# Optimization experiments

Hardware: AMD Instinct MI355X
Metric: run time of the kernel (lower is better)

## Reference

```python
import jax, jax.numpy as jnp
import numpy as np

N = 30000          # num nodes
E = 480000         # num edges (avg degree 16)
K = 3              # Chebyshev filter order
IN = 128           # input feature dim
LAMBDA_MAX = 2.0   # PyG default spectral bound
DIMS = [IN, 16, 32, 64, 128, 256, 512]


def setup_inputs() -> dict:
    key = jax.random.key(0)
    ks = jax.random.split(key, 20)
    inp = {
        "x": jax.random.normal(ks[0], (N, IN), dtype=jnp.float32),
        "edge_index": jax.random.randint(ks[1], (2, E), 0, N, dtype=jnp.int32),
        "edge_weight": jax.random.uniform(ks[2], (E,), dtype=jnp.float32),
        "batch": jnp.arange(N, dtype=jnp.int32),  # each node its own graph -> pooling is identity
    }
    for i in range(6):
        fi, fo = DIMS[i], DIMS[i + 1]
        scale = 1.0 / np.sqrt(fi * K)
        inp[f"W{i+1}"] = jax.random.normal(ks[3 + 2 * i], (K, fi, fo), dtype=jnp.float32) * scale
        inp[f"b{i+1}"] = jnp.zeros((fo,), dtype=jnp.float32)
    inp["fc_w"] = jax.random.normal(ks[16], (512, 3), dtype=jnp.float32) * 0.05
    inp["fc_b"] = jnp.zeros((3,), dtype=jnp.float32)
    return inp


def _cheb_conv(x, row, col, w_off, diag, W, b):
    """ChebConv with rw-normalized, rescaled Laplacian Lhat = 2L/lmax - I.
    Lhat @ v = scatter(w_off * v[row] -> col) + diag * v."""
    def lmv(v):
        return jax.ops.segment_sum(w_off[:, None] * v[row], col, num_segments=N) + diag * v
    Tx0 = x
    out = Tx0 @ W[0]
    Tx1 = lmv(x)
    out = out + Tx1 @ W[1]
    for k in range(2, W.shape[0]):
        Tx2 = 2.0 * lmv(Tx1) - Tx0
        out = out + Tx2 @ W[k]
        Tx0, Tx1 = Tx1, Tx2
    return out + b


def _forward(x, edge_index, edge_weight, batch, Ws, bs, fc_w, fc_b):
    row, col = edge_index[0], edge_index[1]
    # random-walk Laplacian L = I - D^{-1} A, then Lhat = 2L/lmax - I
    deg = jax.ops.segment_sum(edge_weight, row, num_segments=N)
    deg_inv = jnp.where(deg > 0, 1.0 / deg, 0.0)
    w_off = -(2.0 / LAMBDA_MAX) * deg_inv[row] * edge_weight   # off-diagonal entries of Lhat
    diag = 2.0 / LAMBDA_MAX - 1.0                               # diagonal entry of Lhat (0 for lmax=2)
    h = x
    for W, b in zip(Ws, bs):
        h = _cheb_conv(h, row, col, w_off, diag, W, b)
        h = jax.ops.segment_max(h, batch, num_segments=N)  # global_max_pool; identity since batch=arange
        h = jax.nn.softplus(h)
    return h @ fc_w + fc_b


def reference(x, edge_index, edge_weight, batch, W1, b1, W2, b2, W3, b3, W4, b4, W5, b5, W6, b6, fc_w, fc_b):
    Ws = [W1, W2, W3, W4, W5, W6]
    bs = [b1, b2, b3, b4, b5, b6]
    return _forward(x, edge_index, edge_weight, batch, Ws, bs, fc_w, fc_b)
```

## Files before the change

### kernel.cpp

```cpp
#include <hip/hip_runtime.h>
#include <math.h>
#include <stdint.h>

#define NN 30000
#define EE 480000
#define MPAD 30080
#define NPAD 30720
#define NB_HIST 32
#define CHUNK 15000

typedef __attribute__((ext_vector_type(8))) short short8;
typedef __attribute__((ext_vector_type(4))) float floatx4;

__device__ __forceinline__ float b2f(ushort u) {
    union { uint u; float f; } c; c.u = ((uint)u) << 16; return c.f;
}
__device__ __forceinline__ ushort f2b(float f) {
    union { float f; uint u; } c; c.f = f;
    uint u = c.u;
    uint r = (u + 0x7FFFu + ((u >> 16) & 1u)) >> 16;
    return (ushort)r;
}
__device__ __forceinline__ float softplus_f(float x) {
    float a = fabsf(x) * 1.44269504f;
    float t = __builtin_amdgcn_exp2f(-a);
    float l = __builtin_amdgcn_logf(1.f + t);
    return fmaxf(x, 0.f) + 0.69314718f * l;
}

__device__ __forceinline__ void gld_lds16(const void* g, void* lds) {
    __builtin_amdgcn_global_load_lds(
        (__attribute__((address_space(1))) void*)(uintptr_t)(g),
        (__attribute__((address_space(3))) void*)(uint32_t)(uintptr_t)(lds),
        16, 0, 0);
}

__device__ __forceinline__ void barrier_raw() {
    __asm__ volatile("s_barrier" ::: "memory");
}
template <int N>
__device__ __forceinline__ void waitcnt_vm() {
    if constexpr (N == 0) __asm__ volatile("s_waitcnt vmcnt(0)" ::: "memory");
    else if constexpr (N == 2) __asm__ volatile("s_waitcnt vmcnt(2)" ::: "memory");
    else if constexpr (N == 3) __asm__ volatile("s_waitcnt vmcnt(3)" ::: "memory");
    else if constexpr (N == 4) __asm__ volatile("s_waitcnt vmcnt(4)" ::: "memory");
    else if constexpr (N == 8) __asm__ volatile("s_waitcnt vmcnt(8)" ::: "memory");
}


__global__ __launch_bounds__(256) void pre1_fused(
        const int* __restrict__ row, const int* __restrict__ col,
        const float* __restrict__ ew,
        int* __restrict__ Hpart, float* __restrict__ Dpart,
        const float* __restrict__ x, ushort* __restrict__ xb,
        const float* __restrict__ W1, const float* __restrict__ W2,
        const float* __restrict__ W3, const float* __restrict__ W4,
        const float* __restrict__ W5, const float* __restrict__ W6,
        ushort* __restrict__ B1, ushort* __restrict__ B2,
        ushort* __restrict__ B3, ushort* __restrict__ B4,
        ushort* __restrict__ B5, ushort* __restrict__ B6) {
    __shared__ int hist[NPAD];
    int b = blockIdx.x;
    int t = threadIdx.x;
    if (b < NB_HIST) {
        int e0 = b * CHUNK, e1 = e0 + CHUNK;
        #pragma unroll
        for (int i = 0; i < NPAD / 1024; ++i)
            *(int4*)(&hist[(i * 256 + t) * 4]) = make_int4(0, 0, 0, 0);
        __syncthreads();
        int e = e0 + t;
        for (; e + 2048 <= e1; e += 2048) {
            int c0 = col[e],        c1 = col[e + 256];
            int c2 = col[e + 512],  c3 = col[e + 768];
            int c4 = col[e + 1024], c5 = col[e + 1280];
            int c6 = col[e + 1536], c7 = col[e + 1792];
            atomicAdd(&hist[c0], 1); atomicAdd(&hist[c1], 1);
            atomicAdd(&hist[c2], 1); atomicAdd(&hist[c3], 1);
            atomicAdd(&hist[c4], 1); atomicAdd(&hist[c5], 1);
            atomicAdd(&hist[c6], 1); atomicAdd(&hist[c7], 1);
        }
        for (; e < e1; e += 256) atomicAdd(&hist[col[e]], 1);
        __syncthreads();
        #pragma unroll
        for (int i = 0; i < NPAD / 1024; ++i)
            *(int4*)(&Hpart[(size_t)b * NPAD + (i * 256 + t) * 4]) =
                *(const int4*)(&hist[(i * 256 + t) * 4]);
        __syncthreads();
        float* histf = (float*)hist;
        #pragma unroll
        for (int i = 0; i < NPAD / 1024; ++i)
            *(float4*)(&histf[(i * 256 + t) * 4]) = make_float4(0.f, 0.f, 0.f, 0.f);
        __syncthreads();
        e = e0 + t;
        for (; e + 1024 <= e1; e += 1024) {
            int r0 = row[e],       r1 = row[e + 256];
            int r2 = row[e + 512], r3 = row[e + 768];
            float w0 = ew[e],       w1 = ew[e + 256];
            float w2 = ew[e + 512], w3 = ew[e + 768];
            atomicAdd(&histf[r0], w0); atomicAdd(&histf[r1], w1);
            atomicAdd(&histf[r2], w2); atomicAdd(&histf[r3], w3);
        }
        for (; e < e1; e += 256) atomicAdd(&histf[row[e]], ew[e]);
        __syncthreads();
        #pragma unroll
        for (int i = 0; i < NPAD / 1024; ++i)
            *(float4*)(&Dpart[(size_t)b * NPAD + (i * 256 + t) * 4]) =
                *(const float4*)(&histf[(i * 256 + t) * 4]);
    } else if (b < NB_HIST + 480) {
        int id = b - NB_HIST;
        #pragma unroll
        for (int i = 0; i < 8; ++i) {
            int idx = id * 2048 + i * 256 + t;
            if (idx < NN * 128 / 4) {
                float4 v = *(const float4*)(x + (size_t)idx * 4);
                ushort4 o;
                o.x = f2b(v.x); o.y = f2b(v.y); o.z = f2b(v.z); o.w = f2b(v.w);
                *(ushort4*)(xb + (size_t)idx * 4) = o;
            }
        }
    } else {
        int id = b - NB_HIST - 480;
        #pragma unroll
        for (int i = 0; i < 8; ++i) {
            int idx = id * 2048 + i * 256 + t;
            if (idx < 6144) {
                int r = idx >> 7, k = idx & 127;
                int j = r >> 4, n = r & 15;
                B1[idx] = f2b(W1[(j * 128 + k) * 16 + n]);
            } else if (idx < 8192) {
                int tt = idx - 6144; int n = tt >> 6, k = tt & 63;
                B2[tt] = f2b(k < 48 ? W2[k * 32 + n] : 0.f);
            } else if (idx < 14336) {
                int tt = idx - 8192; int n = tt / 96, k = tt - n * 96;
                B3[tt] = f2b(W3[k * 64 + n]);
            } else if (idx < 38912) {
                int tt = idx - 14336; int n = tt / 192, k = tt - n * 192;
                B4[tt] = f2b(W4[k * 128 + n]);
            } else if (idx < 137216) {
                int tt = idx - 38912; int n = tt / 384, k = tt - n * 384;
                B5[tt] = f2b(W5[k * 256 + n]);
            } else if (idx < 530432) {
                int tt = idx - 137216; int n = tt / 768, k = tt - n * 768;
                B6[tt] = f2b(W6[k * 512 + n]);
            }
        }
    }
}

__global__ __launch_bounds__(256) void col_reduce(
        int* __restrict__ Hpart, const float* __restrict__ Dpart,
        int* __restrict__ counts, float* __restrict__ deg) {
    int c = blockIdx.x * 256 + threadIdx.x;
    int run = 0;
    #pragma unroll
    for (int b = 0; b < NB_HIST; ++b) {
        int v = Hpart[(size_t)b * NPAD + c];
        Hpart[(size_t)b * NPAD + c] = run;
        run += v;
    }
    counts[c] = run;
    float s = 0.f;
    #pragma unroll
    for (int b = 0; b < NB_HIST; ++b) s += Dpart[(size_t)b * NPAD + c];
    deg[c] = s;
}

__global__ __launch_bounds__(1024) void scan_one(
        const int* __restrict__ counts, int* __restrict__ offs) {
    __shared__ int ws[16];
    int t = threadIdx.x;
    int wave = t >> 6, lane = t & 63;
    int base = t * 32;
    int c[32];
    int s = 0;
    if (base < NN) {
        #pragma unroll
        for (int g = 0; g < 8; ++g) {
            int4 v = *(const int4*)(counts + base + g * 4);
            c[g * 4 + 0] = v.x; c[g * 4 + 1] = v.y;
            c[g * 4 + 2] = v.z; c[g * 4 + 3] = v.w;
        }
        #pragma unroll
        for (int i = 0; i < 32; ++i) s += c[i];
    } else {
        #pragma unroll
        for (int i = 0; i < 32; ++i) c[i] = 0;
    }
    int incl = s;
    #pragma unroll
    for (int off = 1; off < 64; off <<= 1) {
        int xv = __shfl_up(incl, off);
        if (lane >= off) incl += xv;
    }
    if (lane == 63) ws[wave] = incl;
    __syncthreads();
    if (wave == 0) {
        int v = (lane < 16) ? ws[lane] : 0;
        #pragma unroll
        for (int off = 1; off < 16; off <<= 1) {
            int xv = __shfl_up(v, off);
            if (lane >= off) v += xv;
        }
        if (lane < 16) ws[lane] = v;
    }
    __syncthreads();
    int wbase = (wave == 0) ? 0 : ws[wave - 1];
    int run = wbase + incl - s;
    if (base < NN) {
        int o[32];
        #pragma unroll
        for (int i = 0; i < 32; ++i) { o[i] = run; run += c[i]; }
        #pragma unroll
        for (int g = 0; g < 8; ++g) {
            int4 v = make_int4(o[g * 4], o[g * 4 + 1], o[g * 4 + 2], o[g * 4 + 3]);
            *(int4*)(offs + base + g * 4) = v;
        }
    }
    if (t == 0) offs[NN] = EE;
}

template <int BN, bool ACT>
__device__ __forceinline__ void gemm_mfma_body(
        int bid, const ushort* __restrict__ A, int lda, int K,
        const ushort* __restrict__ Bt, const float* __restrict__ bias,
        ushort* __restrict__ Out, int ldo) {
    constexpr int BM = 128, BK = 32;
    constexpr int SM = 32;
    constexpr int FM = 2;
    constexpr int FN = BN / 16;
    constexpr int CB = BN / 16;
    constexpr int WAITN = (BN == 64) ? 3 : 2;
    __shared__ __align__(16) ushort As[2][BM][BK];
    __shared__ __align__(16) ushort Bs[2][BN][BK];
    int tid = threadIdx.x;
    int wv = tid >> 6, ln = tid & 63;
    int q = ln >> 4, r16 = ln & 15;
    int m0 = bid * BM;

    int lrow = ln >> 2;
    int gseg = (ln & 3) ^ ((ln >> 3) & 3);
    const ushort* Abase = A + (size_t)(m0 + lrow) * lda + gseg * 8;
    const ushort* Bbase = Bt + (size_t)lrow * K + gseg * 8;

    floatx4 acc[FM][FN];
    #pragma unroll
    for (int i = 0; i < FM; ++i)
        #pragma unroll
        for (int j = 0; j < FN; ++j) acc[i][j] = (floatx4){0.f, 0.f, 0.f, 0.f};

    int sw = (q ^ ((r16 >> 1) & 3)) * 8;
    int aoff[FM], boff[FN];
    #pragma unroll
    for (int i = 0; i < FM; ++i) aoff[i] = (wv * SM + i * 16 + r16) * BK + sw;
    #pragma unroll
    for (int j = 0; j < FN; ++j) boff[j] = (j * 16 + r16) * BK + sw;

    auto stage = [&](int b, int k0) {
        gld_lds16(Abase + (size_t)(wv * 16) * lda + k0, &As[b][wv * 16][0]);
        gld_lds16(Abase + (size_t)(64 + wv * 16) * lda + k0, &As[b][64 + wv * 16][0]);
        if constexpr (CB == 4) {
            gld_lds16(Bbase + (size_t)(wv * 16) * K + k0, &Bs[b][wv * 16][0]);
        } else {
            if (wv < CB) gld_lds16(Bbase + (size_t)(wv * 16) * K + k0, &Bs[b][wv * 16][0]);
        }
    };
    auto compute = [&](int b) {
        const ushort* ldsA = &As[b][0][0];
        const ushort* ldsB = &Bs[b][0][0];
        short8 af[FM], bf[FN];
        #pragma unroll
        for (int i = 0; i < FM; ++i) af[i] = *(const short8*)(ldsA + aoff[i]);
        #pragma unroll
        for (int j = 0; j < FN; ++j) bf[j] = *(const short8*)(ldsB + boff[j]);
        #pragma unroll
        for (int i = 0; i < FM; ++i)
            #pragma unroll
            for (int j = 0; j < FN; ++j)
                acc[i][j] = __builtin_amdgcn_mfma_f32_16x16x32_bf16(
                    af[i], bf[j], acc[i][j], 0, 0, 0);
    };

    int nIter = K / BK;
    stage(0, 0);
    for (int i = 0; i < nIter; ++i) {
        int cur = i & 1;
        barrier_raw();
        if (i + 1 < nIter) {
            stage(cur ^ 1, (i + 1) * BK);
            waitcnt_vm<WAITN>();
        } else {
            waitcnt_vm<0>();
        }
        barrier_raw();
        compute(cur);
    }
    #pragma unroll
    for (int i = 0; i < FM; ++i) {
        #pragma unroll
        for (int j = 0; j < FN; ++j) {
            int n = j * 16 + r16;
            float bv = ACT ? bias[n] : 0.f;
            #pragma unroll
            for (int r = 0; r < 4; ++r) {
                int m = m0 + wv * SM + i * 16 + q * 4 + r;
                float v = acc[i][j][r] + bv;
                Out[(size_t)m * ldo + n] = f2b(ACT ? softplus_f(v) : v);
            }
        }
    }
}

template <int BN, bool ACT = true>
__global__ __launch_bounds__(256) void gemm_mfma(
        const ushort* __restrict__ A, int lda, int K,
        const ushort* __restrict__ Bt,
        const float* __restrict__ bias,
        ushort* __restrict__ Out, int ldo) {
    gemm_mfma_body<BN, ACT>(blockIdx.x, A, lda, K, Bt, bias, Out, ldo);
}

__global__ __launch_bounds__(256) void pre2_fused(
        const int* __restrict__ row, const int* __restrict__ col,
        const float* __restrict__ ew, const float* __restrict__ deg,
        const int* __restrict__ offs, const int* __restrict__ Hpart,
        int2* __restrict__ csr_rw,
        const ushort* __restrict__ xb, const ushort* __restrict__ Bt1,
        ushort* __restrict__ Ybuf) {
    int b = blockIdx.x;
    if (b < NB_HIST) {
        __shared__ int cur[NPAD];
        int t = threadIdx.x;
        #pragma unroll
        for (int i = 0; i < NPAD / 1024; ++i) {
            int idx = (i * 256 + t) * 4;
            int4 o = *(const int4*)(offs + idx);
            int4 pfx = *(const int4*)(Hpart + (size_t)b * NPAD + idx);
            cur[idx + 0] = o.x + pfx.x;
            cur[idx + 1] = o.y + pfx.y;
            cur[idx + 2] = o.z + pfx.z;
            cur[idx + 3] = o.w + pfx.w;
        }
        __syncthreads();
        int e0 = b * CHUNK, e1 = e0 + CHUNK;
        int e = e0 + t;
        for (; e + 1024 <= e1; e += 1024) {
            int r0 = row[e],       r1 = row[e + 256];
            int r2 = row[e + 512], r3 = row[e + 768];
            int c0 = col[e],       c1 = col[e + 256];
            int c2 = col[e + 512], c3 = col[e + 768];
            float w0 = ew[e],       w1 = ew[e + 256];
            float w2 = ew[e + 512], w3 = ew[e + 768];
            float d0 = deg[r0], d1 = deg[r1], d2 = deg[r2], d3 = deg[r3];
            float v0 = (d0 > 0.f) ? (-w0 / d0) : 0.f;
            float v1 = (d1 > 0.f) ? (-w1 / d1) : 0.f;
            float v2 = (d2 > 0.f) ? (-w2 / d2) : 0.f;
            float v3 = (d3 > 0.f) ? (-w3 / d3) : 0.f;
            int p0 = atomicAdd(&cur[c0], 1);
            int p1 = atomicAdd(&cur[c1], 1);
            int p2 = atomicAdd(&cur[c2], 1);
            int p3 = atomicAdd(&cur[c3], 1);
            csr_rw[p0] = make_int2(r0, __float_as_int(v0));
            csr_rw[p1] = make_int2(r1, __float_as_int(v1));
            csr_rw[p2] = make_int2(r2, __float_as_int(v2));
            csr_rw[p3] = make_int2(r3, __float_as_int(v3));
        }
        for (; e < e1; e += 256) {
            int r = row[e];
            float d = deg[r];
            float wv = (d > 0.f) ? (-ew[e] / d) : 0.f;
            int pos = atomicAdd(&cur[col[e]], 1);
            csr_rw[pos] = make_int2(r, __float_as_int(wv));
        }
    } else {
        gemm_mfma_body<48, false>(b - NB_HIST, xb, 128, 128, Bt1, nullptr,
                                  Ybuf, 48);
    }
}

template <int FI>
__global__ __launch_bounds__(256) void lmv_bf16(
        const ushort* __restrict__ A, ushort* __restrict__ Out,
        const ushort* __restrict__ Sub, int ldi, int ldo,
        const int* __restrict__ offs, const int2* __restrict__ rw,
        float scale, int N) {
    constexpr int NPW = 64 / FI;
    int wave = threadIdx.x >> 6;
    int lane = threadIdx.x & 63;
    int sub = lane / FI;
    int fbase = lane & (FI - 1);
    int node = blockIdx.x * (4 * NPW) + wave * NPW + sub;
    if (node >= N) return;
    int e0 = offs[node], e1 = offs[node + 1];
    float acc[4];
    #pragma unroll
    for (int c = 0; c < 4; ++c) acc[c] = 0.f;
    int e = e0;
    for (; e + 4 <= e1; e += 4) {
        int2 u0 = rw[e], u1 = rw[e + 1], u2 = rw[e + 2], u3 = rw[e + 3];
        acc[0] += __int_as_float(u0.y) * b2f(A[(size_t)u0.x * ldi + fbase]);
        acc[1] += __int_as_float(u1.y) * b2f(A[(size_t)u1.x * ldi + fbase]);
        acc[2] += __int_as_float(u2.y) * b2f(A[(size_t)u2.x * ldi + fbase]);
        acc[3] += __int_as_float(u3.y) * b2f(A[(size_t)u3.x * ldi + fbase]);
    }
    for (; e < e1; ++e) {
        int2 u = rw[e];
        acc[0] += __int_as_float(u.y) * b2f(A[(size_t)u.x * ldi + fbase]);
    }
    float a = (acc[0] + acc[1]) + (acc[2] + acc[3]);
    ushort* o = Out + (size_t)node * ldo + fbase;
    if (Sub) {
        const ushort* s = Sub + (size_t)node * ldo + fbase;
        *o = f2b(scale * a - b2f(*s));
    } else {
        *o = f2b(scale * a);
    }
}

__global__ __launch_bounds__(256) void lmv_l1_final(
        const ushort* __restrict__ Z,
        const ushort* __restrict__ Y,
        const float* __restrict__ b,
        ushort* __restrict__ Out,
        const int* __restrict__ offs, const int2* __restrict__ rw, int N) {
    int wave = threadIdx.x >> 6;
    int lane = threadIdx.x & 63;
    int sub = lane >> 4, f = lane & 15;
    int node = blockIdx.x * 16 + wave * 4 + sub;
    if (node >= N) return;
    int e0 = offs[node], e1 = offs[node + 1];
    const ushort* Z2 = Z + 16;
    float acc[4];
    #pragma unroll
    for (int c = 0; c < 4; ++c) acc[c] = 0.f;
    int e = e0;
    for (; e + 4 <= e1; e += 4) {
        int2 u0 = rw[e], u1 = rw[e + 1], u2 = rw[e + 2], u3 = rw[e + 3];
        acc[0] += __int_as_float(u0.y) * b2f(Z2[(size_t)u0.x * 32 + f]);
        acc[1] += __int_as_float(u1.y) * b2f(Z2[(size_t)u1.x * 32 + f]);
        acc[2] += __int_as_float(u2.y) * b2f(Z2[(size_t)u2.x * 32 + f]);
        acc[3] += __int_as_float(u3.y) * b2f(Z2[(size_t)u3.x * 32 + f]);
    }
    for (; e < e1; ++e) {
        int2 u = rw[e];
        acc[0] += __int_as_float(u.y) * b2f(Z2[(size_t)u.x * 32 + f]);
    }
    float z3 = (acc[0] + acc[1]) + (acc[2] + acc[3]);
    float y0 = b2f(Y[(size_t)node * 48 + f]);
    float y2 = b2f(Y[(size_t)node * 48 + 32 + f]);
    float z1 = b2f(Z[(size_t)node * 32 + f]);
    float v = y0 + z1 + 2.f * z3 - y2 + b[f];
    Out[(size_t)node * 64 + f] = f2b(softplus_f(v));
}

template <int LPG>
__global__ __launch_bounds__(256) void lmv_grp(
        const ushort* __restrict__ A, ushort* __restrict__ Out,
        const ushort* __restrict__ Sub, int ld,
        const int* __restrict__ offs, const int2* __restrict__ rw,
        float scale) {
    constexpr int EG = 64 / LPG;
    int node = blockIdx.x * 4 + (threadIdx.x >> 6);
    int lane = threadIdx.x & 63;
    int g = lane / LPG;
    int li = lane % LPG;
    int fbase = li * 4;
    int e0 = __builtin_amdgcn_readfirstlane(offs[node]);
    int e1 = __builtin_amdgcn_readfirstlane(offs[node + 1]);
    float a0[4], a1[4];
    #pragma unroll
    for (int j = 0; j < 4; ++j) { a0[j] = 0.f; a1[j] = 0.f; }
    int e = e0 + g;
    for (; e + EG < e1; e += 2 * EG) {
        int2 u0 = rw[e];
        int2 u1 = rw[e + EG];
        float w0 = __int_as_float(u0.y), w1 = __int_as_float(u1.y);
        ushort4 v0 = *(const ushort4*)(A + (size_t)u0.x * ld + fbase);
        ushort4 v1 = *(const ushort4*)(A + (size_t)u1.x * ld + fbase);
        a0[0] += w0 * b2f(v0.x); a0[1] += w0 * b2f(v0.y);
        a0[2] += w0 * b2f(v0.z); a0[3] += w0 * b2f(v0.w);
        a1[0] += w1 * b2f(v1.x); a1[1] += w1 * b2f(v1.y);
        a1[2] += w1 * b2f(v1.z); a1[3] += w1 * b2f(v1.w);
    }
    if (e < e1) {
        int2 u = rw[e];
        float w = __int_as_float(u.y);
        ushort4 v = *(const ushort4*)(A + (size_t)u.x * ld + fbase);
        a0[0] += w * b2f(v.x); a0[1] += w * b2f(v.y);
        a0[2] += w * b2f(v.z); a0[3] += w * b2f(v.w);
    }
    #pragma unroll
    for (int j = 0; j < 4; ++j) {
        float a = a0[j] + a1[j];
        #pragma unroll
        for (int off = LPG; off < 64; off <<= 1)
            a += __shfl_xor(a, off);
        a0[j] = a;
    }
    if (g == 0) {
        ushort* o = Out + (size_t)node * ld + fbase;
        ushort4 w;
        if (Sub) {
            ushort4 s = *(const ushort4*)(Sub + (size_t)node * ld + fbase);
            w.x = f2b(scale * a0[0] - b2f(s.x));
            w.y = f2b(scale * a0[1] - b2f(s.y));
            w.z = f2b(scale * a0[2] - b2f(s.z));
            w.w = f2b(scale * a0[3] - b2f(s.w));
        } else {
            w.x = f2b(scale * a0[0]); w.y = f2b(scale * a0[1]);
            w.z = f2b(scale * a0[2]); w.w = f2b(scale * a0[3]);
        }
        *(ushort4*)o = w;
    }
}

template <int VEC>
__global__ __launch_bounds__(256) void lmv_vec(
        const ushort* __restrict__ A, ushort* __restrict__ Out,
        const ushort* __restrict__ Sub, int ld,
        const int* __restrict__ offs, const int2* __restrict__ rw,
        float scale) {
    constexpr int CH = 8;
    int node = blockIdx.x * 4 + (threadIdx.x >> 6);
    int lane = threadIdx.x & 63;
    int fbase = lane * VEC;
    int e0 = __builtin_amdgcn_readfirstlane(offs[node]);
    int e1 = __builtin_amdgcn_readfirstlane(offs[node + 1]);
    float acc[CH][VEC];
    #pragma unroll
    for (int c = 0; c < CH; ++c)
        #pragma unroll
        for (int v = 0; v < VEC; ++v) acc[c][v] = 0.f;
    int e = e0;
    for (; e + CH <= e1; e += CH) {
        #pragma unroll
        for (int c = 0; c < CH; ++c) {
            int2 u = rw[e + c];
            int r = u.x;
            float we = __int_as_float(u.y);
            const ushort* pr = A + (size_t)r * ld + fbase;
            if constexpr (VEC == 4) {
                ushort4 uu = *(const ushort4*)pr;
                acc[c][0] += we * b2f(uu.x); acc[c][1] += we * b2f(uu.y);
                acc[c][2] += we * b2f(uu.z); acc[c][3] += we * b2f(uu.w);
            } else if constexpr (VEC == 2) {
                ushort2 uu = *(const ushort2*)pr;
                acc[c][0] += we * b2f(uu.x); acc[c][1] += we * b2f(uu.y);
            } else {
                acc[c][0] += we * b2f(*pr);
            }
        }
    }
    for (; e < e1; ++e) {
        int c = e & (CH - 1);
        int2 u = rw[e];
        int r = u.x;
        float we = __int_as_float(u.y);
        const ushort* pr = A + (size_t)r * ld + fbase;
        if constexpr (VEC == 4) {
            ushort4 uu = *(const ushort4*)pr;
            acc[c][0] += we * b2f(uu.x); acc[c][1] += we * b2f(uu.y);
            acc[c][2] += we * b2f(uu.z); acc[c][3] += we * b2f(uu.w);
        } else if constexpr (VEC == 2) {
            ushort2 uu = *(const ushort2*)pr;
            acc[c][0] += we * b2f(uu.x); acc[c][1] += we * b2f(uu.y);
        } else {
            acc[c][0] += we * b2f(*pr);
        }
    }
    #pragma unroll
    for (int c = 1; c < CH; ++c)
        #pragma unroll
        for (int v = 0; v < VEC; ++v) acc[0][v] += acc[c][v];
    ushort* o = Out + (size_t)node * ld + fbase;
    if (Sub) {
        const ushort* s = Sub + (size_t)node * ld + fbase;
        ushort tmp[VEC];
        #pragma unroll
        for (int v = 0; v < VEC; ++v) tmp[v] = f2b(scale * acc[0][v] - b2f(s[v]));
        #pragma unroll
        for (int v = 0; v < VEC; ++v) o[v] = tmp[v];
    } else {
        #pragma unroll
        for (int v = 0; v < VEC; ++v) o[v] = f2b(scale * acc[0][v]);
    }
}

template <bool FC = false, int YB = 0>
__global__ __launch_bounds__(256) void gemm_bk64(
        const ushort* __restrict__ A, int lda, int K,
        const ushort* __restrict__ Bt,
        const float* __restrict__ bias,
        ushort* __restrict__ Out, int ldo,
        const float* __restrict__ fcw, float* __restrict__ fcout) {
    constexpr int BM = 128, BN = 128, BK = 64;
    __shared__ __align__(16) ushort As[2][BM][BK];
    __shared__ __align__(16) ushort Bs[2][BN][BK];
    int tid = threadIdx.x;
    int wv = tid >> 6, ln = tid & 63;
    int wm = wv & 1, wn = wv >> 1;
    int q = ln >> 4, r16 = ln & 15;
    int nwg = gridDim.x;
    int orig = blockIdx.x;
    int xcd = orig & 7;
    int qq = nwg >> 3, rr = nwg & 7;
    int wbase = (xcd < rr) ? xcd * (qq + 1) : rr * (qq + 1) + (xcd - rr) * qq;
    int wgid = wbase + (orig >> 3);
    int yb = wgid & ((1 << YB) - 1);
    int xb = wgid >> YB;
    int m0 = xb * BM;
    int n0 = yb * BN;

    int lrow8 = ln >> 3, slds = ln & 7;
    int gseg = slds ^ lrow8;
    const ushort* Abase = A + (size_t)(m0 + lrow8) * lda + gseg * 8;
    const ushort* Bbase = Bt + (size_t)(n0 + lrow8) * K + gseg * 8;

    floatx4 acc[4][4];
    #pragma unroll
    for (int i = 0; i < 4; ++i)
        #pragma unroll
        for (int j = 0; j < 4; ++j) acc[i][j] = (floatx4){0.f, 0.f, 0.f, 0.f};

    int r7 = r16 & 7;
    int aoff[2][4], boff[2][4];
    #pragma unroll
    for (int s = 0; s < 2; ++s) {
        int segp = ((s * 4 + q) ^ r7) * 8;
        #pragma unroll
        for (int i = 0; i < 4; ++i) {
            aoff[s][i] = (wm * 64 + i * 16 + r16) * BK + segp;
            boff[s][i] = (wn * 64 + i * 16 + r16) * BK + segp;
        }
    }

    auto stage = [&](int b, int k0) {
        #pragma unroll
        for (int g = 0; g < 4; ++g)
            gld_lds16(Abase + (size_t)(wv * 8 + g * 32) * lda + k0,
                      &As[b][wv * 8 + g * 32][0]);
        #pragma unroll
        for (int g = 0; g < 4; ++g)
            gld_lds16(Bbase + (size_t)(wv * 8 + g * 32) * K + k0,
                      &Bs[b][wv * 8 + g * 32][0]);
    };
    auto compute = [&](int b) {
        const ushort* ldsA = &As[b][0][0];
        const ushort* ldsB = &Bs[b][0][0];
        #pragma unroll
        for (int s = 0; s < 2; ++s) {
            short8 af[4], bf[4];
            #pragma unroll
            for (int i = 0; i < 4; ++i) af[i] = *(const short8*)(ldsA + aoff[s][i]);
            #pragma unroll
            for (int j = 0; j < 4; ++j) bf[j] = *(const short8*)(ldsB + boff[s][j]);
            #pragma unroll
            for (int i = 0; i < 4; ++i)
                #pragma unroll
                for (int j = 0; j < 4; ++j)
                    acc[i][j] = __builtin_amdgcn_mfma_f32_16x16x32_bf16(
                        af[i], bf[j], acc[i][j], 0, 0, 0);
        }
    };

    int nIter = K / BK;
    stage(0, 0);
    for (int i = 0; i < nIter; ++i) {
        int cur = i & 1;
        barrier_raw();
        if (i + 1 < nIter) {
            stage(cur ^ 1, (i + 1) * BK);
            waitcnt_vm<8>();
        } else {
            waitcnt_vm<0>();
        }
        barrier_raw();
        compute(cur);
    }

    if constexpr (FC) {
        int pb = yb * 2 + wn;
        #pragma unroll
        for (int i = 0; i < 4; ++i) {
            #pragma unroll
            for (int r = 0; r < 4; ++r) {
                float p0 = 0.f, p1 = 0.f, p2 = 0.f;
                #pragma unroll
                for (int j = 0; j < 4; ++j) {
                    int n = n0 + wn * 64 + j * 16 + r16;
                    float v = softplus_f(acc[i][j][r] + bias[n]);
                    p0 += v * fcw[n * 3 + 0];
                    p1 += v * fcw[n * 3 + 1];
                    p2 += v * fcw[n * 3 + 2];
                }
                #pragma unroll
                for (int off = 1; off < 16; off <<= 1) {
                    p0 += __shfl_xor(p0, off);
                    p1 += __shfl_xor(p1, off);
                    p2 += __shfl_xor(p2, off);
                }
                if (r16 == 0) {
                    int m = m0 + wm * 64 + i * 16 + q * 4 + r;
                    float* dst = fcout + ((size_t)pb * MPAD + m) * 3;
                    dst[0] = p0; dst[1] = p1; dst[2] = p2;
                }
            }
        }
    } else {
        #pragma unroll
        for (int i = 0; i < 4; ++i) {
            #pragma unroll
            for (int j = 0; j < 4; ++j) {
                int n = n0 + wn * 64 + j * 16 + r16;
                float bv = bias[n];
                #pragma unroll
                for (int r = 0; r < 4; ++r) {
                    int m = m0 + wm * 64 + i * 16 + q * 4 + r;
                    Out[(size_t)m * ldo + n] = f2b(softplus_f(acc[i][j][r] + bv));
                }
            }
        }
    }
}

__global__ __launch_bounds__(256) void fc_reduce(
        const float* __restrict__ part, const float* __restrict__ fcb,
        float* __restrict__ out) {
    int idx = blockIdx.x * blockDim.x + threadIdx.x;
    if (idx >= NN * 3) return;
    int c = idx - (idx / 3) * 3;
    float s = 0.f;
    #pragma unroll
    for (int pb = 0; pb < 8; ++pb)
        s += part[(size_t)pb * MPAD * 3 + idx];
    out[idx] = s + fcb[c];
}

static inline size_t align256(size_t x) { return (x + 255) & ~(size_t)255; }

extern "C" void kernel_launch(void* const* d_in, const int* in_sizes, int n_in,
                              void* d_out, int out_size, void* d_ws, size_t ws_size,
                              hipStream_t stream) {
    const float* x   = (const float*)d_in[0];
    const int*   ei  = (const int*)d_in[1];
    const float* ew  = (const float*)d_in[2];
    const float* W[6]  = { (const float*)d_in[4],  (const float*)d_in[6],
                           (const float*)d_in[8],  (const float*)d_in[10],
                           (const float*)d_in[12], (const float*)d_in[14] };
    const float* Bv[6] = { (const float*)d_in[5],  (const float*)d_in[7],
                           (const float*)d_in[9],  (const float*)d_in[11],
                           (const float*)d_in[13], (const float*)d_in[15] };
    const float* fc_w = (const float*)d_in[16];
    const float* fc_b = (const float*)d_in[17];
    float* out = (float*)d_out;

    const int* e_row = ei;
    const int* e_col = ei + EE;

    const int fi_arr[5]   = { 16, 32, 64, 128, 256 };
    const int fo_arr[5]   = { 32, 64, 128, 256, 512 };
    const int Kpad_arr[5] = { 64, 96, 192, 384, 768 };
    const int ldo_arr[5]  = { 96, 192, 384, 768, 512 };

    char* p = (char*)d_ws;
    float* deg    = (float*)p; p += align256((size_t)NPAD * 4);
    int*   counts = (int*)p;   p += align256((size_t)NPAD * 4);
    int*   offs   = (int*)p;   p += align256((size_t)(NPAD + 4) * 4);
    int*   Hpart  = (int*)p;   p += align256((size_t)NB_HIST * NPAD * 4);
    float* Dpart  = (float*)p; p += align256((size_t)NB_HIST * NPAD * 4);
    int2*  csr_rw = (int2*)p;  p += align256((size_t)EE * 8);
    ushort* Bt1   = (ushort*)p; p += align256((size_t)48 * 128 * 2);
    ushort* Bt[5];
    for (int L = 0; L < 5; ++L) {
        Bt[L] = (ushort*)p;
        p += align256((size_t)fo_arr[L] * Kpad_arr[L] * 2);
    }
    float* fcpart = (float*)p; p += align256((size_t)8 * MPAD * 3 * 4);
    ushort* xb   = (ushort*)p; p += align256((size_t)MPAD * 128 * 2);
    ushort* Ybuf = (ushort*)p; p += align256((size_t)MPAD * 48 * 2);
    ushort* Zbuf = (ushort*)p; p += align256((size_t)MPAD * 32 * 2);
    ushort* buf0 = (ushort*)p; p += align256((size_t)MPAD * 768 * 2);
    ushort* buf1 = (ushort*)p; p += align256((size_t)MPAD * 768 * 2);
    (void)ws_size; (void)n_in; (void)in_sizes; (void)out_size;


    pre1_fused<<<NB_HIST + 480 + 260, 256, 0, stream>>>(
        e_row, e_col, ew, Hpart, Dpart, x, xb,
        W[0], W[1], W[2], W[3], W[4], W[5],
        Bt1, Bt[0], Bt[1], Bt[2], Bt[3], Bt[4]);

    col_reduce<<<NPAD / 256, 256, 0, stream>>>(Hpart, Dpart, counts, deg);

    scan_one<<<1, 1024, 0, stream>>>(counts, offs);

    pre2_fused<<<NB_HIST + MPAD / 128, 256, 0, stream>>>(
        e_row, e_col, ew, deg, offs, Hpart, csr_rw, xb, Bt1, Ybuf);

    lmv_bf16<32><<<(NN + 7) / 8, 256, 0, stream>>>(
        Ybuf + 16, Zbuf, nullptr, 48, 32, offs, csr_rw, 1.0f, NN);
    lmv_l1_final<<<(NN + 15) / 16, 256, 0, stream>>>(
        Zbuf, Ybuf, Bv[0], buf1, offs, csr_rw, NN);

    ushort* Abuf[5] = { buf1, buf0, buf1, buf0, buf1 };
    ushort* Obuf[5] = { buf0, buf1, buf0, buf1, buf0 };

    for (int L = 0; L < 5; ++L) {
        int fi = fi_arr[L];
        int ldA = Kpad_arr[L];
        int ldO = ldo_arr[L];
        ushort* A = Abuf[L];
        ushort* O = Obuf[L];

        switch (fi) {
            case 16:
                lmv_bf16<16><<<(NN + 15) / 16, 256, 0, stream>>>(
                    A, A + fi, nullptr, ldA, ldA, offs, csr_rw, 1.0f, NN);
                lmv_bf16<16><<<(NN + 15) / 16, 256, 0, stream>>>(
                    A + fi, A + 2 * fi, A, ldA, ldA, offs, csr_rw, 2.0f, NN);
                break;
            case 32:
                lmv_bf16<32><<<(NN + 7) / 8, 256, 0, stream>>>(
                    A, A + fi, nullptr, ldA, ldA, offs, csr_rw, 1.0f, NN);
                lmv_bf16<32><<<(NN + 7) / 8, 256, 0, stream>>>(
                    A + fi, A + 2 * fi, A, ldA, ldA, offs, csr_rw, 2.0f, NN);
                break;
            case 64:
                lmv_grp<16><<<NN / 4, 256, 0, stream>>>(
                    A, A + fi, nullptr, ldA, offs, csr_rw, 1.0f);
                lmv_grp<16><<<NN / 4, 256, 0, stream>>>(
                    A + fi, A + 2 * fi, A, ldA, offs, csr_rw, 2.0f);
                break;
            case 128:
                lmv_grp<32><<<NN / 4, 256, 0, stream>>>(
                    A, A + fi, nullptr, ldA, offs, csr_rw, 1.0f);
                lmv_grp<32><<<NN / 4, 256, 0, stream>>>(
                    A + fi, A + 2 * fi, A, ldA, offs, csr_rw, 2.0f);
                break;
            default:
                lmv_vec<4><<<NN / 4, 256, 0, stream>>>(
                    A, A + fi, nullptr, ldA, offs, csr_rw, 1.0f);
                lmv_vec<4><<<NN / 4, 256, 0, stream>>>(
                    A + fi, A + 2 * fi, A, ldA, offs, csr_rw, 2.0f);
                break;
        }

        int K = Kpad_arr[L];
        switch (fo_arr[L]) {
            case 32:
                gemm_mfma<32><<<dim3(MPAD / 128), 256, 0, stream>>>(
                    A, ldA, K, Bt[L], Bv[L + 1], O, ldO);
                break;
            case 64:
                gemm_mfma<64><<<dim3(MPAD / 128), 256, 0, stream>>>(
                    A, ldA, K, Bt[L], Bv[L + 1], O, ldO);
                break;
            case 128:
                gemm_bk64<false, 0><<<dim3(MPAD / 128), 256, 0, stream>>>(
                    A, ldA, K, Bt[L], Bv[L + 1], O, ldO, nullptr, nullptr);
                break;
            case 256:
                gemm_bk64<false, 1><<<dim3(MPAD / 128 * 2), 256, 0, stream>>>(
                    A, ldA, K, Bt[L], Bv[L + 1], O, ldO, nullptr, nullptr);
                break;
            default:
                gemm_bk64<true, 2><<<dim3(MPAD / 128 * 4), 256, 0, stream>>>(
                    A, ldA, K, Bt[L], Bv[L + 1], nullptr, 0, fc_w, fcpart);
                break;
        }
    }

    fc_reduce<<<(NN * 3 + 255) / 256, 256, 0, stream>>>(fcpart, fc_b, out);
}
```

Measured before the change: 459.9 us.

## Split feature columns into 64-wide chunks pinned to XCDs for L2 locality

Replaces the vectorized per-node SpMM kernel for the 128- and 256-wide layers with a chunked kernel. Each 64-column slice of the feature matrix is assigned to a subset of XCDs via the block index modulo 8, so each XCD's L2 only caches a slice of the gathered rows. Edge list loads and output stores become nontemporal. This gives up vector loads (each lane now loads a single bf16) and per-node unrolling depth, and relies on the round-robin mapping of blocks to XCDs.

```diff
diff --git a/kernel.cpp b/kernel.cpp
--- a/kernel.cpp
+++ b/kernel.cpp
@@ -513,75 +513,56 @@
     }
 }
 
-template <int VEC>
-__global__ __launch_bounds__(256) void lmv_vec(
+template <int NCHUNK>
+__global__ __launch_bounds__(256) void lmv_chunk(
         const ushort* __restrict__ A, ushort* __restrict__ Out,
         const ushort* __restrict__ Sub, int ld,
         const int* __restrict__ offs, const int2* __restrict__ rw,
         float scale) {
-    constexpr int CH = 8;
-    int node = blockIdx.x * 4 + (threadIdx.x >> 6);
+    constexpr int XPC = 8 / NCHUNK;
+    int b = blockIdx.x;
+    int xcd = b & 7;
+    int chunk = xcd / XPC;
+    int rank = (b >> 3) * XPC + (xcd % XPC);
+    if (rank >= 1875) return;
+    int coff = chunk * 64;
+    int wave = threadIdx.x >> 6;
     int lane = threadIdx.x & 63;
-    int fbase = lane * VEC;
-    int e0 = __builtin_amdgcn_readfirstlane(offs[node]);
-    int e1 = __builtin_amdgcn_readfirstlane(offs[node + 1]);
-    float acc[CH][VEC];
-    #pragma unroll
-    for (int c = 0; c < CH; ++c)
-        #pragma unroll
-        for (int v = 0; v < VEC; ++v) acc[c][v] = 0.f;
-    int e = e0;
-    for (; e + CH <= e1; e += CH) {
-        #pragma unroll
-        for (int c = 0; c < CH; ++c) {
-            int2 u = rw[e + c];
-            int r = u.x;
-            float we = __int_as_float(u.y);
-            const ushort* pr = A + (size_t)r * ld + fbase;
-            if constexpr (VEC == 4) {
-                ushort4 uu = *(const ushort4*)pr;
-                acc[c][0] += we * b2f(uu.x); acc[c][1] += we * b2f(uu.y);
-                acc[c][2] += we * b2f(uu.z); acc[c][3] += we * b2f(uu.w);
-            } else if constexpr (VEC == 2) {
-                ushort2 uu = *(const ushort2*)pr;
-                acc[c][0] += we * b2f(uu.x); acc[c][1] += we * b2f(uu.y);
-            } else {
-                acc[c][0] += we * b2f(*pr);
-            }
-        }
-    }
-    for (; e < e1; ++e) {
-        int c = e & (CH - 1);
-        int2 u = rw[e];
-        int r = u.x;
-        float we = __int_as_float(u.y);
-        const ushort* pr = A + (size_t)r * ld + fbase;
-        if constexpr (VEC == 4) {
-            ushort4 uu = *(const ushort4*)pr;
-            acc[c][0] += we * b2f(uu.x); acc[c][1] += we * b2f(uu.y);
-            acc[c][2] += we * b2f(uu.z); acc[c][3] += we * b2f(uu.w);
-        } else if constexpr (VEC == 2) {
-            ushort2 uu = *(const ushort2*)pr;
-            acc[c][0] += we * b2f(uu.x); acc[c][1] += we * b2f(uu.y);
+    const ushort* Ac = A + coff + lane;
+    #pragma unroll
+    for (int nn = 0; nn < 4; ++nn) {
+        int node = rank * 16 + wave * 4 + nn;
+        int e0 = offs[node], e1 = offs[node + 1];
+        float ac0 = 0.f, ac1 = 0.f, ac2 = 0.f, ac3 = 0.f;
+        int e = e0;
+        for (; e + 4 <= e1; e += 4) {
+            long long q0 = __builtin_nontemporal_load((const long long*)(rw + e));
+            long long q1 = __builtin_nontemporal_load((const long long*)(rw + e + 1));
+            long long q2 = __builtin_nontemporal_load((const long long*)(rw + e + 2));
+            long long q3 = __builtin_nontemporal_load((const long long*)(rw + e + 3));
+            int r0 = (int)q0; float w0 = __int_as_float((int)(q0 >> 32));
+            int r1 = (int)q1; float w1 = __int_as_float((int)(q1 >> 32));
+            int r2 = (int)q2; float w2 = __int_as_float((int)(q2 >> 32));
+            int r3 = (int)q3; float w3 = __int_as_float((int)(q3 >> 32));
+            ac0 += w0 * b2f(Ac[(size_t)r0 * ld]);
+            ac1 += w1 * b2f(Ac[(size_t)r1 * ld]);
+            ac2 += w2 * b2f(Ac[(size_t)r2 * ld]);
+            ac3 += w3 * b2f(Ac[(size_t)r3 * ld]);
+        }
+        for (; e < e1; ++e) {
+            long long q = __builtin_nontemporal_load((const long long*)(rw + e));
+            int r = (int)q; float w = __int_as_float((int)(q >> 32));
+            ac0 += w * b2f(Ac[(size_t)r * ld]);
+        }
+        float a = (ac0 + ac1) + (ac2 + ac3);
+        ushort ov;
+        if (Sub) {
+            ushort sv = Sub[(size_t)node * ld + coff + lane];
+            ov = f2b(scale * a - b2f(sv));
         } else {
-            acc[c][0] += we * b2f(*pr);
-        }
-    }
-    #pragma unroll
-    for (int c = 1; c < CH; ++c)
-        #pragma unroll
-        for (int v = 0; v < VEC; ++v) acc[0][v] += acc[c][v];
-    ushort* o = Out + (size_t)node * ld + fbase;
-    if (Sub) {
-        const ushort* s = Sub + (size_t)node * ld + fbase;
-        ushort tmp[VEC];
-        #pragma unroll
-        for (int v = 0; v < VEC; ++v) tmp[v] = f2b(scale * acc[0][v] - b2f(s[v]));
-        #pragma unroll
-        for (int v = 0; v < VEC; ++v) o[v] = tmp[v];
-    } else {
-        #pragma unroll
-        for (int v = 0; v < VEC; ++v) o[v] = f2b(scale * acc[0][v]);
+            ov = f2b(scale * a);
+        }
+        __builtin_nontemporal_store(ov, Out + (size_t)node * ld + coff + lane);
     }
 }
 
@@ -830,15 +811,15 @@
                     A + fi, A + 2 * fi, A, ldA, offs, csr_rw, 2.0f);
                 break;
             case 128:
-                lmv_grp<32><<<NN / 4, 256, 0, stream>>>(
+                lmv_chunk<2><<<8 * 469, 256, 0, stream>>>(
                     A, A + fi, nullptr, ldA, offs, csr_rw, 1.0f);
-                lmv_grp<32><<<NN / 4, 256, 0, stream>>>(
+                lmv_chunk<2><<<8 * 469, 256, 0, stream>>>(
                     A + fi, A + 2 * fi, A, ldA, offs, csr_rw, 2.0f);
                 break;
             default:
-                lmv_vec<4><<<NN / 4, 256, 0, stream>>>(
+                lmv_chunk<4><<<8 * 938, 256, 0, stream>>>(
                     A, A + fi, nullptr, ldA, offs, csr_rw, 1.0f);
-                lmv_vec<4><<<NN / 4, 256, 0, stream>>>(
+                lmv_chunk<4><<<8 * 938, 256, 0, stream>>>(
                     A + fi, A + 2 * fi, A, ldA, offs, csr_rw, 2.0f);
                 break;
         }
```

After: 632.0 us. +37.4%, slower.

## Switch large GEMMs to 4-stage BK=32 pipelined LDS prefetch

Applied to the files above, without the earlier changes.

Replaces the double-buffered BK=64 GEMM with a four-buffer BK=32 pipeline that prefetches three k-steps ahead using direct global-to-LDS loads. The staging layout and XOR swizzle change to match the narrower 32-element rows. The aim is to hide global load latency with more loads in flight while keeping the same LDS footprint. The cost is twice as many barriers per unit of K and less MFMA work between syncs.

```diff
diff --git a/kernel.cpp b/kernel.cpp
--- a/kernel.cpp
+++ b/kernel.cpp
@@ -45,6 +45,7 @@
     else if constexpr (N == 3) __asm__ volatile("s_waitcnt vmcnt(3)" ::: "memory");
     else if constexpr (N == 4) __asm__ volatile("s_waitcnt vmcnt(4)" ::: "memory");
     else if constexpr (N == 8) __asm__ volatile("s_waitcnt vmcnt(8)" ::: "memory");
+    else if constexpr (N == 12) __asm__ volatile("s_waitcnt vmcnt(12)" ::: "memory");
 }
 
 
@@ -585,16 +586,16 @@
     }
 }
 
-template <bool FC = false, int YB = 0>
-__global__ __launch_bounds__(256) void gemm_bk64(
+template <bool FC, int YB>
+__global__ __launch_bounds__(256) void gemm_pipe(
         const ushort* __restrict__ A, int lda, int K,
         const ushort* __restrict__ Bt,
         const float* __restrict__ bias,
         ushort* __restrict__ Out, int ldo,
         const float* __restrict__ fcw, float* __restrict__ fcout) {
-    constexpr int BM = 128, BN = 128, BK = 64;
-    __shared__ __align__(16) ushort As[2][BM][BK];
-    __shared__ __align__(16) ushort Bs[2][BN][BK];
+    constexpr int BM = 128, BN = 128, BK = 32;
+    __shared__ __align__(16) ushort As[4][BM][BK];
+    __shared__ __align__(16) ushort Bs[4][BN][BK];
     int tid = threadIdx.x;
     int wv = tid >> 6, ln = tid & 63;
     int wm = wv & 1, wn = wv >> 1;
@@ -610,10 +611,10 @@
     int m0 = xb * BM;
     int n0 = yb * BN;
 
-    int lrow8 = ln >> 3, slds = ln & 7;
-    int gseg = slds ^ lrow8;
-    const ushort* Abase = A + (size_t)(m0 + lrow8) * lda + gseg * 8;
-    const ushort* Bbase = Bt + (size_t)(n0 + lrow8) * K + gseg * 8;
+    int lrow = ln >> 2;
+    int gseg = (ln & 3) ^ ((ln >> 3) & 3);
+    const ushort* Abase = A + (size_t)(m0 + lrow) * lda + gseg * 8;
+    const ushort* Bbase = Bt + (size_t)(n0 + lrow) * K + gseg * 8;
 
     floatx4 acc[4][4];
     #pragma unroll
@@ -621,55 +622,50 @@
         #pragma unroll
         for (int j = 0; j < 4; ++j) acc[i][j] = (floatx4){0.f, 0.f, 0.f, 0.f};
 
-    int r7 = r16 & 7;
-    int aoff[2][4], boff[2][4];
-    #pragma unroll
-    for (int s = 0; s < 2; ++s) {
-        int segp = ((s * 4 + q) ^ r7) * 8;
-        #pragma unroll
-        for (int i = 0; i < 4; ++i) {
-            aoff[s][i] = (wm * 64 + i * 16 + r16) * BK + segp;
-            boff[s][i] = (wn * 64 + i * 16 + r16) * BK + segp;
-        }
+    int sw = (q ^ ((r16 >> 1) & 3)) * 8;
+    int aoff[4], boff[4];
+    #pragma unroll
+    for (int i = 0; i < 4; ++i) {
+        aoff[i] = (wm * 64 + i * 16 + r16) * BK + sw;
+        boff[i] = (wn * 64 + i * 16 + r16) * BK + sw;
     }
 
     auto stage = [&](int b, int k0) {
-        #pragma unroll
-        for (int g = 0; g < 4; ++g)
-            gld_lds16(Abase + (size_t)(wv * 8 + g * 32) * lda + k0,
-                      &As[b][wv * 8 + g * 32][0]);
-        #pragma unroll
-        for (int g = 0; g < 4; ++g)
-            gld_lds16(Bbase + (size_t)(wv * 8 + g * 32) * K + k0,
-                      &Bs[b][wv * 8 + g * 32][0]);
+        gld_lds16(Abase + (size_t)(wv * 16) * lda + k0, &As[b][wv * 16][0]);
+        gld_lds16(Abase + (size_t)(64 + wv * 16) * lda + k0, &As[b][64 + wv * 16][0]);
+        gld_lds16(Bbase + (size_t)(wv * 16) * K + k0, &Bs[b][wv * 16][0]);
+        gld_lds16(Bbase + (size_t)(64 + wv * 16) * K + k0, &Bs[b][64 + wv * 16][0]);
     };
     auto compute = [&](int b) {
         const ushort* ldsA = &As[b][0][0];
         const ushort* ldsB = &Bs[b][0][0];
-        #pragma unroll
-        for (int s = 0; s < 2; ++s) {
-            short8 af[4], bf[4];
+        short8 af[4], bf[4];
+        #pragma unroll
+        for (int i = 0; i < 4; ++i) af[i] = *(const short8*)(ldsA + aoff[i]);
+        #pragma unroll
+        for (int j = 0; j < 4; ++j) bf[j] = *(const short8*)(ldsB + boff[j]);
+        #pragma unroll
+        for (int i = 0; i < 4; ++i)
             #pragma unroll
-            for (int i = 0; i < 4; ++i) af[i] = *(const short8*)(ldsA + aoff[s][i]);
-            #pragma unroll
-            for (int j = 0; j < 4; ++j) bf[j] = *(const short8*)(ldsB + boff[s][j]);
-            #pragma unroll
-            for (int i = 0; i < 4; ++i)
-                #pragma unroll
-                for (int j = 0; j < 4; ++j)
-                    acc[i][j] = __builtin_amdgcn_mfma_f32_16x16x32_bf16(
-                        af[i], bf[j], acc[i][j], 0, 0, 0);
-        }
+            for (int j = 0; j < 4; ++j)
+                acc[i][j] = __builtin_amdgcn_mfma_f32_16x16x32_bf16(
+                    af[i], bf[j], acc[i][j], 0, 0, 0);
     };
 
     int nIter = K / BK;
     stage(0, 0);
+    stage(1, BK);
+    stage(2, 2 * BK);
     for (int i = 0; i < nIter; ++i) {
-        int cur = i & 1;
+        int cur = i & 3;
         barrier_raw();
-        if (i + 1 < nIter) {
-            stage(cur ^ 1, (i + 1) * BK);
+        if (i + 3 < nIter) {
+            stage((i + 3) & 3, (i + 3) * BK);
+            waitcnt_vm<12>();
+        } else if (i + 2 < nIter) {
             waitcnt_vm<8>();
+        } else if (i + 1 < nIter) {
+            waitcnt_vm<4>();
         } else {
             waitcnt_vm<0>();
         }
@@ -854,15 +850,15 @@
                     A, ldA, K, Bt[L], Bv[L + 1], O, ldO);
                 break;
             case 128:
-                gemm_bk64<false, 0><<<dim3(MPAD / 128), 256, 0, stream>>>(
+                gemm_pipe<false, 0><<<dim3(MPAD / 128), 256, 0, stream>>>(
                     A, ldA, K, Bt[L], Bv[L + 1], O, ldO, nullptr, nullptr);
                 break;
             case 256:
-                gemm_bk64<false, 1><<<dim3(MPAD / 128 * 2), 256, 0, stream>>>(
+                gemm_pipe<false, 1><<<dim3(MPAD / 128 * 2), 256, 0, stream>>>(
                     A, ldA, K, Bt[L], Bv[L + 1], O, ldO, nullptr, nullptr);
                 break;
             default:
-                gemm_bk64<true, 2><<<dim3(MPAD / 128 * 4), 256, 0, stream>>>(
+                gemm_pipe<true, 2><<<dim3(MPAD / 128 * 4), 256, 0, stream>>>(
                     A, ldA, K, Bt[L], Bv[L + 1], nullptr, 0, fc_w, fcpart);
                 break;
         }
```

After: 464.6 us. Within noise of the previous version (+1.0%).

## Fuse second Chebyshev Laplacian gather into GEMM prologue for mid layers

Applied to the files above, without the earlier changes.

For the layers with input width 64 and 128, the launch computing Tx2 = 2·L·Tx1 − Tx0 is removed. Each GEMM block now computes Tx2 for its own 128 rows in a prologue, using a shuffle-reduced CSR gather, then runs the matrix multiply. This drops one launch per layer and one round trip of Tx2 through memory. The cost is that the gather runs with only one GEMM-sized grid of 4-wave blocks, far less parallelism than the standalone kernel. In the 256-output layer, the two column blocks sharing a row tile both compute and write the same Tx2 rows, which doubles that work.

```diff
diff --git a/kernel.cpp b/kernel.cpp
--- a/kernel.cpp
+++ b/kernel.cpp
@@ -585,13 +585,14 @@
     }
 }
 
-template <bool FC = false, int YB = 0>
+template <bool FC, int YB, int FUSE_FI>
 __global__ __launch_bounds__(256) void gemm_bk64(
         const ushort* __restrict__ A, int lda, int K,
         const ushort* __restrict__ Bt,
         const float* __restrict__ bias,
         ushort* __restrict__ Out, int ldo,
-        const float* __restrict__ fcw, float* __restrict__ fcout) {
+        const float* __restrict__ fcw, float* __restrict__ fcout,
+        const int* __restrict__ offs, const int2* __restrict__ rw) {
     constexpr int BM = 128, BN = 128, BK = 64;
     __shared__ __align__(16) ushort As[2][BM][BK];
     __shared__ __align__(16) ushort Bs[2][BN][BK];
@@ -609,6 +610,64 @@
     int xb = wgid >> YB;
     int m0 = xb * BM;
     int n0 = yb * BN;
+
+    if constexpr (FUSE_FI > 0) {
+        constexpr int LPG = FUSE_FI / 4;
+        constexpr int EG = 64 / LPG;
+        int g = ln / LPG, li = ln % LPG;
+        int fb = li * 4;
+        const ushort* T1 = A + FUSE_FI;
+        const ushort* T0 = A;
+        ushort* T2 = const_cast<ushort*>(A) + 2 * FUSE_FI;
+        for (int rr2 = 0; rr2 < 32; ++rr2) {
+            int node = m0 + wv * 32 + rr2;
+            if (node < NN) {
+                int e0 = __builtin_amdgcn_readfirstlane(offs[node]);
+                int e1 = __builtin_amdgcn_readfirstlane(offs[node + 1]);
+                float a0[4], a1[4];
+                #pragma unroll
+                for (int j = 0; j < 4; ++j) { a0[j] = 0.f; a1[j] = 0.f; }
+                int e = e0 + g;
+                for (; e + EG < e1; e += 2 * EG) {
+                    int2 u0 = rw[e];
+                    int2 u1 = rw[e + EG];
+                    float w0 = __int_as_float(u0.y), w1 = __int_as_float(u1.y);
+                    ushort4 v0 = *(const ushort4*)(T1 + (size_t)u0.x * lda + fb);
+                    ushort4 v1 = *(const ushort4*)(T1 + (size_t)u1.x * lda + fb);
+                    a0[0] += w0 * b2f(v0.x); a0[1] += w0 * b2f(v0.y);
+                    a0[2] += w0 * b2f(v0.z); a0[3] += w0 * b2f(v0.w);
+                    a1[0] += w1 * b2f(v1.x); a1[1] += w1 * b2f(v1.y);
+                    a1[2] += w1 * b2f(v1.z); a1[3] += w1 * b2f(v1.w);
+                }
+                if (e < e1) {
+                    int2 u = rw[e];
+                    float w = __int_as_float(u.y);
+                    ushort4 v = *(const ushort4*)(T1 + (size_t)u.x * lda + fb);
+                    a0[0] += w * b2f(v.x); a0[1] += w * b2f(v.y);
+                    a0[2] += w * b2f(v.z); a0[3] += w * b2f(v.w);
+                }
+                #pragma unroll
+                for (int j = 0; j < 4; ++j) {
+                    float a = a0[j] + a1[j];
+                    #pragma unroll
+                    for (int off = LPG; off < 64; off <<= 1)
+                        a += __shfl_xor(a, off);
+                    a0[j] = a;
+                }
+                if (g == 0) {
+                    ushort4 s = *(const ushort4*)(T0 + (size_t)node * lda + fb);
+                    ushort4 o;
+                    o.x = f2b(2.f * a0[0] - b2f(s.x));
+                    o.y = f2b(2.f * a0[1] - b2f(s.y));
+                    o.z = f2b(2.f * a0[2] - b2f(s.z));
+                    o.w = f2b(2.f * a0[3] - b2f(s.w));
+                    *(ushort4*)(T2 + (size_t)node * lda + fb) = o;
+                }
+            }
+        }
+        waitcnt_vm<0>();
+        barrier_raw();
+    }
 
     int lrow8 = ln >> 3, slds = ln & 7;
     int gseg = slds ^ lrow8;
@@ -826,14 +885,10 @@
             case 64:
                 lmv_grp<16><<<NN / 4, 256, 0, stream>>>(
                     A, A + fi, nullptr, ldA, offs, csr_rw, 1.0f);
-                lmv_grp<16><<<NN / 4, 256, 0, stream>>>(
-                    A + fi, A + 2 * fi, A, ldA, offs, csr_rw, 2.0f);
                 break;
             case 128:
                 lmv_grp<32><<<NN / 4, 256, 0, stream>>>(
                     A, A + fi, nullptr, ldA, offs, csr_rw, 1.0f);
-                lmv_grp<32><<<NN / 4, 256, 0, stream>>>(
-                    A + fi, A + 2 * fi, A, ldA, offs, csr_rw, 2.0f);
                 break;
             default:
                 lmv_vec<4><<<NN / 4, 256, 0, stream>>>(
@@ -854,16 +909,19 @@
                     A, ldA, K, Bt[L], Bv[L + 1], O, ldO);
                 break;
             case 128:
-                gemm_bk64<false, 0><<<dim3(MPAD / 128), 256, 0, stream>>>(
-                    A, ldA, K, Bt[L], Bv[L + 1], O, ldO, nullptr, nullptr);
+                gemm_bk64<false, 0, 64><<<dim3(MPAD / 128), 256, 0, stream>>>(
+                    A, ldA, K, Bt[L], Bv[L + 1], O, ldO, nullptr, nullptr,
+                    offs, csr_rw);
                 break;
             case 256:
-                gemm_bk64<false, 1><<<dim3(MPAD / 128 * 2), 256, 0, stream>>>(
-                    A, ldA, K, Bt[L], Bv[L + 1], O, ldO, nullptr, nullptr);
+                gemm_bk64<false, 1, 128><<<dim3(MPAD / 128 * 2), 256, 0, stream>>>(
+                    A, ldA, K, Bt[L], Bv[L + 1], O, ldO, nullptr, nullptr,
+                    offs, csr_rw);
                 break;
             default:
-                gemm_bk64<true, 2><<<dim3(MPAD / 128 * 4), 256, 0, stream>>>(
-                    A, ldA, K, Bt[L], Bv[L + 1], nullptr, 0, fc_w, fcpart);
+                gemm_bk64<true, 2, 0><<<dim3(MPAD / 128 * 4), 256, 0, stream>>>(
+                    A, ldA, K, Bt[L], Bv[L + 1], nullptr, 0, fc_w, fcpart,
+                    offs, csr_rw);
                 break;
         }
     }
```

After: 596.8 us. 29.8% more time.
